# Optimization experiments

Measured on AMD Instinct MI355X. Metric: run time of the kernel, lower is better.

## Reference

```python
import jax, jax.numpy as jnp
import numpy as np

N_NODES = 100000
N_EDGES = 1600000
IN_FEATS = 128
OUT_FEATS = 128


def setup_inputs() -> dict:
    key = jax.random.key(0)
    k1, k2, k3, k4, k5, k6, k7 = jax.random.split(key, 7)
    feat = jax.random.normal(k1, (N_NODES, IN_FEATS), dtype=jnp.float32)
    # positive per-node norms (sqrt-degree-like), shifted away from zero
    in_norm = jax.random.uniform(k2, (N_NODES,), dtype=jnp.float32) + 0.5
    out_norm = jax.random.uniform(k3, (N_NODES,), dtype=jnp.float32) + 0.5
    src = jax.random.randint(k4, (N_EDGES,), 0, N_NODES, dtype=jnp.int32)
    dst = jax.random.randint(k5, (N_EDGES,), 0, N_NODES, dtype=jnp.int32)
    # linear params, uniform(-stdv, stdv) as in reset_parameters
    stdv = 1.0 / np.sqrt(IN_FEATS)
    W = jax.random.uniform(k6, (OUT_FEATS, IN_FEATS), dtype=jnp.float32, minval=-stdv, maxval=stdv)
    b = jax.random.uniform(k7, (OUT_FEATS,), dtype=jnp.float32, minval=-stdv, maxval=stdv)
    return {"feat": feat, "in_norm": in_norm, "out_norm": out_norm,
            "src": src, "dst": dst, "W": W, "b": b}


def reference(feat, in_norm, out_norm, src, dst, W, b):
    # h_u = feat / out_norm  (per source node)
    h = feat / out_norm[:, None]                      # [N, F]
    # copy_u + sum: scatter-add source features into destination nodes
    msgs = h[src]                                     # [E, F] gather
    agg = jax.ops.segment_sum(msgs, dst, num_segments=N_NODES)  # [N, F]
    # normalize by in_norm, then linear
    out = (agg / in_norm[:, None]) @ W.T + b          # [N, F_out]
    return out
```

## Files before the change

kernel.cpp:

```cpp
#include <hip/hip_runtime.h>

#define N_NODES 100000
#define N_EDGES 1600000
#define F 128
#define NB2 391
#define BSZ 256
#define CHUNK 4000
#define NBLK_BIN 400
#define CAP2 5440
#define NGROUP 6250

#define WS_V7 32627712

typedef __attribute__((ext_vector_type(8))) short short8;
typedef __attribute__((ext_vector_type(4))) float f32x4;

__device__ __forceinline__ unsigned short f2bf(float f) {
    unsigned u = __float_as_uint(f);
    return (unsigned short)((u + 0x7fffu + ((u >> 16) & 1u)) >> 16);
}

__global__ __launch_bounds__(256) void prep_chist_kernel(
    const float* __restrict__ feat, const float* __restrict__ out_norm,
    const int* __restrict__ dst,
    unsigned short* __restrict__ h, int* __restrict__ base_t)
{
    __shared__ int c[NB2];
    const int t = threadIdx.x;
    const bool do_hist = (blockIdx.x < NBLK_BIN);
    if (do_hist) {
        for (int i = t; i < NB2; i += 256) c[i] = 0;
        __syncthreads();
    }
    int q = blockIdx.x * 256 + t;
    int row = q >> 5;
    float r = 1.0f / out_norm[row];
    float4 v = ((const float4*)feat)[q];
    ushort4 o;
    o.x = f2bf(v.x * r); o.y = f2bf(v.y * r);
    o.z = f2bf(v.z * r); o.w = f2bf(v.w * r);
    ((ushort4*)h)[q] = o;
    if (do_hist) {
        int e0 = blockIdx.x * CHUNK;
        for (int i = t; i < CHUNK; i += 256)
            atomicAdd(&c[dst[e0 + i] >> 8], 1);
        __syncthreads();
        for (int i = t; i < NB2; i += 256)
            base_t[i * NBLK_BIN + blockIdx.x] = c[i];
    }
}

__global__ __launch_bounds__(64) void cscan1_kernel(
    int* __restrict__ base_t, int* __restrict__ btot)
{
    int b = blockIdx.x, l = threadIdx.x;
    int carry = 0;
    #pragma unroll
    for (int r = 0; r < 7; ++r) {
        int idx = r * 64 + l;
        bool ok = idx < NBLK_BIN;
        int v = ok ? base_t[b * NBLK_BIN + idx] : 0;
        int incl = v;
        #pragma unroll
        for (int off = 1; off < 64; off <<= 1) {
            int n = __shfl_up(incl, off);
            if (l >= off) incl += n;
        }
        if (ok) base_t[b * NBLK_BIN + idx] = incl - v + carry;
        carry += __shfl(incl, 63);
    }
    if (l == 0) btot[b] = carry;
}

__global__ __launch_bounds__(512) void binscatter_kernel(
    const int* __restrict__ src, const int* __restrict__ dst,
    const int* __restrict__ base_t, const int* __restrict__ btot,
    int* __restrict__ pool)
{
    __shared__ int cba[NB2];
    __shared__ int sm[512];
    int t = threadIdx.x, blk = blockIdx.x;
    int v = (t < NB2) ? btot[t] : 0;
    sm[t] = v;
    __syncthreads();
    for (int off = 1; off < 512; off <<= 1) {
        int x = (t >= off) ? sm[t - off] : 0;
        __syncthreads();
        sm[t] += x;
        __syncthreads();
    }
    if (t < NB2) cba[t] = (sm[t] - v) + base_t[t * NBLK_BIN + blk];
    __syncthreads();
    int e0 = blk * CHUNK;
    for (int i = t; i < CHUNK; i += 512) {
        int d = dst[e0 + i];
        int s = src[e0 + i];
        int b = d >> 8;
        int pos = atomicAdd(&cba[b], 1);
        pool[pos] = ((d & 255) << 17) | s;
    }
}

__global__ __launch_bounds__(1024) void fsort_gather_kernel(
    const int* __restrict__ pool, const int* __restrict__ btot,
    const unsigned short* __restrict__ h, const float* __restrict__ in_norm,
    float* __restrict__ agg)
{
    __shared__ int pairs[CAP2];
    __shared__ int sorted_s[CAP2];
    __shared__ int fcnt[BSZ];
    __shared__ int s0[BSZ];
    __shared__ int sexcl[BSZ];
    __shared__ int wsum[4];
    __shared__ int woff[4];
    __shared__ int sbeg[1];

    const int t = threadIdx.x, b = blockIdx.x;
    const int lane = t & 63, wv = t >> 6;

    if (t < 64) {
        int acc = 0;
        for (int j = t; j < NB2; j += 64) acc += (j < b) ? btot[j] : 0;
        #pragma unroll
        for (int off = 32; off; off >>= 1) acc += __shfl_xor(acc, off);
        if (t == 0) sbeg[0] = acc;
    }
    if (t < BSZ) fcnt[t] = 0;
    __syncthreads();
    const int beg = sbeg[0];
    int cnt = btot[b];
    if (cnt > CAP2) cnt = CAP2;

    for (int i = t; i < cnt; i += 1024) pairs[i] = pool[beg + i];
    __syncthreads();
    for (int i = t; i < cnt; i += 1024) atomicAdd(&fcnt[pairs[i] >> 17], 1);
    __syncthreads();

    if (t < BSZ) {
        int v = fcnt[t];
        int incl = v;
        #pragma unroll
        for (int off = 1; off < 64; off <<= 1) {
            int n = __shfl_up(incl, off);
            if (lane >= off) incl += n;
        }
        s0[t] = incl;
        if (lane == 63) wsum[wv] = incl;
    }
    __syncthreads();
    if (t < 64) {
        int v = (t < 4) ? wsum[t] : 0;
        int incl = v;
        #pragma unroll
        for (int off = 1; off < 4; off <<= 1) {
            int n = __shfl_up(incl, off);
            if (lane >= off) incl += n;
        }
        if (t < 4) woff[t] = incl - v;
    }
    __syncthreads();
    if (t < BSZ) {
        int sv = s0[t] + woff[t >> 6];
        s0[t] = sv;
        sexcl[t] = sv - fcnt[t];
    }
    __syncthreads();

    for (int i = t; i < cnt; i += 1024) {
        int p = pairs[i];
        int pos = atomicAdd(&sexcl[p >> 17], 1);
        sorted_s[pos] = p & 0x1FFFF;
    }
    __syncthreads();

    const unsigned* hp = (const unsigned*)h;
    const int node0 = b << 8;
    const int nEnd = wv * 16 + 16;
    for (int nl = wv * 16; nl < nEnd; ++nl) {
        const int node = node0 + nl;
        if (node >= N_NODES) break;
        const int start = (nl == 0) ? 0 : s0[nl - 1];
        const int end = s0[nl];
        float ax = 0.f, ay = 0.f;
        int e = start;
        for (; e + 7 < end; e += 8) {
            unsigned u0 = hp[(size_t)sorted_s[e]     * 64 + lane];
            unsigned u1 = hp[(size_t)sorted_s[e + 1] * 64 + lane];
            unsigned u2 = hp[(size_t)sorted_s[e + 2] * 64 + lane];
            unsigned u3 = hp[(size_t)sorted_s[e + 3] * 64 + lane];
            unsigned u4 = hp[(size_t)sorted_s[e + 4] * 64 + lane];
            unsigned u5 = hp[(size_t)sorted_s[e + 5] * 64 + lane];
            unsigned u6 = hp[(size_t)sorted_s[e + 6] * 64 + lane];
            unsigned u7 = hp[(size_t)sorted_s[e + 7] * 64 + lane];
            ax += __uint_as_float(u0 << 16) + __uint_as_float(u1 << 16)
                + __uint_as_float(u2 << 16) + __uint_as_float(u3 << 16)
                + __uint_as_float(u4 << 16) + __uint_as_float(u5 << 16)
                + __uint_as_float(u6 << 16) + __uint_as_float(u7 << 16);
            ay += __uint_as_float(u0 & 0xffff0000u) + __uint_as_float(u1 & 0xffff0000u)
                + __uint_as_float(u2 & 0xffff0000u) + __uint_as_float(u3 & 0xffff0000u)
                + __uint_as_float(u4 & 0xffff0000u) + __uint_as_float(u5 & 0xffff0000u)
                + __uint_as_float(u6 & 0xffff0000u) + __uint_as_float(u7 & 0xffff0000u);
        }
        for (; e + 3 < end; e += 4) {
            unsigned u0 = hp[(size_t)sorted_s[e]     * 64 + lane];
            unsigned u1 = hp[(size_t)sorted_s[e + 1] * 64 + lane];
            unsigned u2 = hp[(size_t)sorted_s[e + 2] * 64 + lane];
            unsigned u3 = hp[(size_t)sorted_s[e + 3] * 64 + lane];
            ax += __uint_as_float(u0 << 16) + __uint_as_float(u1 << 16)
                + __uint_as_float(u2 << 16) + __uint_as_float(u3 << 16);
            ay += __uint_as_float(u0 & 0xffff0000u) + __uint_as_float(u1 & 0xffff0000u)
                + __uint_as_float(u2 & 0xffff0000u) + __uint_as_float(u3 & 0xffff0000u);
        }
        for (; e < end; ++e) {
            unsigned u = hp[(size_t)sorted_s[e] * 64 + lane];
            ax += __uint_as_float(u << 16);
            ay += __uint_as_float(u & 0xffff0000u);
        }
        const float rin = 1.0f / in_norm[node];
        float2 o; o.x = ax * rin; o.y = ay * rin;
        ((float2*)agg)[(size_t)node * 64 + lane] = o;
    }
}

__global__ __launch_bounds__(256) void transform_mfma_kernel(
    float* __restrict__ out, const float* __restrict__ W,
    const float* __restrict__ bias)
{
    __shared__ short Wb[F * F];
    const int t = threadIdx.x;
    #pragma unroll
    for (int i = 0; i < 8; ++i) {
        int c = t + i * 256;
        int n = c >> 4, kc = c & 15;
        const float4* wp = (const float4*)(W + n * F + kc * 8);
        float4 w0 = wp[0], w1 = wp[1];
        short8 v;
        v[0] = (short)f2bf(w0.x); v[1] = (short)f2bf(w0.y);
        v[2] = (short)f2bf(w0.z); v[3] = (short)f2bf(w0.w);
        v[4] = (short)f2bf(w1.x); v[5] = (short)f2bf(w1.y);
        v[6] = (short)f2bf(w1.z); v[7] = (short)f2bf(w1.w);
        *(short8*)&Wb[n * F + ((kc ^ (n & 15)) * 8)] = v;
    }
    __syncthreads();

    const int wave = t >> 6, lane = t & 63;
    const int wblk = blockIdx.x * 4 + wave;
    if (wblk >= NGROUP) return;
    const int r0 = wblk * 16;
    const int m = lane & 15, q = lane >> 4;
    const float4* arow = (const float4*)(out + (size_t)(r0 + m) * F);

    short8 afrag[4];
    #pragma unroll
    for (int s = 0; s < 4; ++s) {
        int k0 = s * 32 + q * 8;
        float4 x0 = arow[k0 >> 2];
        float4 x1 = arow[(k0 >> 2) + 1];
        short8 a;
        a[0] = (short)f2bf(x0.x); a[1] = (short)f2bf(x0.y);
        a[2] = (short)f2bf(x0.z); a[3] = (short)f2bf(x0.w);
        a[4] = (short)f2bf(x1.x); a[5] = (short)f2bf(x1.y);
        a[6] = (short)f2bf(x1.z); a[7] = (short)f2bf(x1.w);
        afrag[s] = a;
    }

    f32x4 acc[8];
    #pragma unroll
    for (int c = 0; c < 8; ++c) { f32x4 z = {0.f, 0.f, 0.f, 0.f}; acc[c] = z; }

    #pragma unroll
    for (int s = 0; s < 4; ++s) {
        const int kc = s * 4 + q;
        #pragma unroll
        for (int c = 0; c < 8; ++c) {
            const int n = c * 16 + m;
            short8 bfrag = *(const short8*)&Wb[n * F + ((kc ^ m) * 8)];
            acc[c] = __builtin_amdgcn_mfma_f32_16x16x32_bf16(
                afrag[s], bfrag, acc[c], 0, 0, 0);
        }
    }

    #pragma unroll
    for (int c = 0; c < 8; ++c) {
        const float bc = bias[c * 16 + m];
        #pragma unroll
        for (int r = 0; r < 4; ++r) {
            out[(size_t)(r0 + q * 4 + r) * F + c * 16 + m] = acc[c][r] + bc;
        }
    }
}

__global__ __launch_bounds__(256) void scatter_kernel(
    const float* __restrict__ feat, const float* __restrict__ out_norm,
    const int* __restrict__ src, const int* __restrict__ dst,
    float* __restrict__ agg)
{
    const int wave = threadIdx.x >> 6;
    const int lane = threadIdx.x & 63;
    const int e = blockIdx.x * 4 + wave;
    const int s = src[e];
    const int d = dst[e];
    const float rn = 1.0f / out_norm[s];
    const float2 v = ((const float2*)(feat + (size_t)s * F))[lane];
    float* ap = agg + (size_t)d * F + lane * 2;
    unsafeAtomicAdd(ap,     v.x * rn);
    unsafeAtomicAdd(ap + 1, v.y * rn);
}

__global__ __launch_bounds__(256) void transform_kernel(
    float* __restrict__ out, const float* __restrict__ in_norm,
    const float* __restrict__ W, const float* __restrict__ bias)
{
    __shared__ float Wt[F * F];
    const int t = threadIdx.x;
    #pragma unroll
    for (int i = 0; i < (F * F) / 256; ++i) {
        int idx = t + i * 256;
        int j = idx >> 7;
        int k = idx & (F - 1);
        Wt[k * F + j] = W[idx];
    }
    __syncthreads();
    const int wave = t >> 6, lane = t & 63;
    const float b0 = bias[lane];
    const float b1 = bias[lane + 64];
    const int ngroups = N_NODES / 16;
    for (int g = blockIdx.x; g < ngroups; g += gridDim.x) {
        const int r = g * 16 + wave * 4;
        const float4* a0 = (const float4*)(out + (size_t)r * F);
        const float4* a1 = a0 + F / 4;
        const float4* a2 = a0 + 2 * (F / 4);
        const float4* a3 = a0 + 3 * (F / 4);
        float acc00 = 0.f, acc01 = 0.f, acc10 = 0.f, acc11 = 0.f;
        float acc20 = 0.f, acc21 = 0.f, acc30 = 0.f, acc31 = 0.f;
        for (int k4 = 0; k4 < F / 4; ++k4) {
            const float4 x0 = a0[k4]; const float4 x1 = a1[k4];
            const float4 x2 = a2[k4]; const float4 x3 = a3[k4];
            const float xs0[4] = {x0.x, x0.y, x0.z, x0.w};
            const float xs1[4] = {x1.x, x1.y, x1.z, x1.w};
            const float xs2[4] = {x2.x, x2.y, x2.z, x2.w};
            const float xs3[4] = {x3.x, x3.y, x3.z, x3.w};
            #pragma unroll
            for (int kk = 0; kk < 4; ++kk) {
                const int k = k4 * 4 + kk;
                const float w0 = Wt[k * F + lane];
                const float w1 = Wt[k * F + 64 + lane];
                acc00 = fmaf(xs0[kk], w0, acc00); acc01 = fmaf(xs0[kk], w1, acc01);
                acc10 = fmaf(xs1[kk], w0, acc10); acc11 = fmaf(xs1[kk], w1, acc11);
                acc20 = fmaf(xs2[kk], w0, acc20); acc21 = fmaf(xs2[kk], w1, acc21);
                acc30 = fmaf(xs3[kk], w0, acc30); acc31 = fmaf(xs3[kk], w1, acc31);
            }
        }
        const float i0 = 1.0f / in_norm[r + 0];
        const float i1 = 1.0f / in_norm[r + 1];
        const float i2 = 1.0f / in_norm[r + 2];
        const float i3 = 1.0f / in_norm[r + 3];
        out[(size_t)(r + 0) * F + lane]      = acc00 * i0 + b0;
        out[(size_t)(r + 0) * F + 64 + lane] = acc01 * i0 + b1;
        out[(size_t)(r + 1) * F + lane]      = acc10 * i1 + b0;
        out[(size_t)(r + 1) * F + 64 + lane] = acc11 * i1 + b1;
        out[(size_t)(r + 2) * F + lane]      = acc20 * i2 + b0;
        out[(size_t)(r + 2) * F + 64 + lane] = acc21 * i2 + b1;
        out[(size_t)(r + 3) * F + lane]      = acc30 * i3 + b0;
        out[(size_t)(r + 3) * F + 64 + lane] = acc31 * i3 + b1;
    }
}

extern "C" void kernel_launch(void* const* d_in, const int* in_sizes, int n_in,
                              void* d_out, int out_size, void* d_ws, size_t ws_size,
                              hipStream_t stream) {
    const float* feat     = (const float*)d_in[0];
    const float* in_norm  = (const float*)d_in[1];
    const float* out_norm = (const float*)d_in[2];
    const int*   src      = (const int*)d_in[3];
    const int*   dst      = (const int*)d_in[4];
    const float* W        = (const float*)d_in[5];
    const float* b        = (const float*)d_in[6];
    float* out = (float*)d_out;

    if (ws_size >= (size_t)WS_V7) {
        char* w = (char*)d_ws;
        int*            pool   = (int*)(w + 0);
        int*            base_t = (int*)(w + 6400000);
        int*            btot   = (int*)(w + 7025600);
        unsigned short* h      = (unsigned short*)(w + 7027712);

        prep_chist_kernel<<<(N_NODES * 32) / 256, 256, 0, stream>>>(
            feat, out_norm, dst, h, base_t);
        cscan1_kernel<<<NB2, 64, 0, stream>>>(base_t, btot);
        binscatter_kernel<<<NBLK_BIN, 512, 0, stream>>>(src, dst, base_t, btot, pool);
        fsort_gather_kernel<<<NB2, 1024, 0, stream>>>(pool, btot, h, in_norm, out);
        transform_mfma_kernel<<<(NGROUP + 3) / 4, 256, 0, stream>>>(out, W, b);
    } else {
        hipMemsetAsync(out, 0, (size_t)N_NODES * F * sizeof(float), stream);
        scatter_kernel<<<N_EDGES / 4, 256, 0, stream>>>(feat, out_norm, src, dst, out);
        transform_kernel<<<2048, 256, 0, stream>>>(out, in_norm, W, b);
    }
}
```

Baseline: 229.7 us.

## Apply linear transform before aggregation and fuse it into the prep kernel

Because the linear layer commutes with the per-node sum, the change multiplies the scaled source features by W (MFMA, bf16) inside the prep/histogram kernel and stores the transformed rows as bf16. The gather kernel then sums transformed rows, scales by in_norm and adds the bias, writing the final output directly. This removes the separate transform kernel and its read and write of the full fp32 aggregate. In exchange the prep kernel carries 32KB of LDS for W and does the GEMM work there, and the output rounding now happens before aggregation.

```diff
diff --git a/kernel.cpp b/kernel.cpp
--- a/kernel.cpp
+++ b/kernel.cpp
@@ -9,8 +9,9 @@
 #define NBLK_BIN 400
 #define CAP2 5440
 #define NGROUP 6250
-
-#define WS_V7 32627712
+#define NPREP_BLK 1563
+
+#define WS_V8 32627712
 
 typedef __attribute__((ext_vector_type(8))) short short8;
 typedef __attribute__((ext_vector_type(4))) float f32x4;
@@ -20,31 +21,88 @@
     return (unsigned short)((u + 0x7fffu + ((u >> 16) & 1u)) >> 16);
 }
 
-__global__ __launch_bounds__(256) void prep_chist_kernel(
+__global__ __launch_bounds__(256) void prep_gemm_chist_kernel(
     const float* __restrict__ feat, const float* __restrict__ out_norm,
-    const int* __restrict__ dst,
-    unsigned short* __restrict__ h, int* __restrict__ base_t)
-{
+    const int* __restrict__ dst, const float* __restrict__ W,
+    unsigned short* __restrict__ g, int* __restrict__ base_t)
+{
+    __shared__ short Wb[F * F];
     __shared__ int c[NB2];
     const int t = threadIdx.x;
     const bool do_hist = (blockIdx.x < NBLK_BIN);
     if (do_hist) {
         for (int i = t; i < NB2; i += 256) c[i] = 0;
-        __syncthreads();
-    }
-    int q = blockIdx.x * 256 + t;
-    int row = q >> 5;
-    float r = 1.0f / out_norm[row];
-    float4 v = ((const float4*)feat)[q];
-    ushort4 o;
-    o.x = f2bf(v.x * r); o.y = f2bf(v.y * r);
-    o.z = f2bf(v.z * r); o.w = f2bf(v.w * r);
-    ((ushort4*)h)[q] = o;
+    }
+    #pragma unroll
+    for (int i = 0; i < 8; ++i) {
+        int cc = t + i * 256;
+        int n = cc >> 4, kc = cc & 15;
+        const float4* wp = (const float4*)(W + n * F + kc * 8);
+        float4 w0 = wp[0], w1 = wp[1];
+        short8 v;
+        v[0] = (short)f2bf(w0.x); v[1] = (short)f2bf(w0.y);
+        v[2] = (short)f2bf(w0.z); v[3] = (short)f2bf(w0.w);
+        v[4] = (short)f2bf(w1.x); v[5] = (short)f2bf(w1.y);
+        v[6] = (short)f2bf(w1.z); v[7] = (short)f2bf(w1.w);
+        *(short8*)&Wb[n * F + ((kc ^ (n & 15)) * 8)] = v;
+    }
+    __syncthreads();
+
     if (do_hist) {
         int e0 = blockIdx.x * CHUNK;
         for (int i = t; i < CHUNK; i += 256)
             atomicAdd(&c[dst[e0 + i] >> 8], 1);
-        __syncthreads();
+    }
+
+    const int wave = t >> 6, lane = t & 63;
+    const int wblk = blockIdx.x * 4 + wave;
+    if (wblk < NGROUP) {
+        const int r0 = wblk * 16;
+        const int m = lane & 15, q = lane >> 4;
+        const float* arow = feat + (size_t)(r0 + m) * F;
+        const float rscale = 1.0f / out_norm[r0 + m];
+
+        short8 afrag[4];
+        #pragma unroll
+        for (int s = 0; s < 4; ++s) {
+            int k0 = s * 32 + q * 8;
+            float4 x0 = *(const float4*)(arow + k0);
+            float4 x1 = *(const float4*)(arow + k0 + 4);
+            short8 a;
+            a[0] = (short)f2bf(x0.x * rscale); a[1] = (short)f2bf(x0.y * rscale);
+            a[2] = (short)f2bf(x0.z * rscale); a[3] = (short)f2bf(x0.w * rscale);
+            a[4] = (short)f2bf(x1.x * rscale); a[5] = (short)f2bf(x1.y * rscale);
+            a[6] = (short)f2bf(x1.z * rscale); a[7] = (short)f2bf(x1.w * rscale);
+            afrag[s] = a;
+        }
+
+        f32x4 acc[8];
+        #pragma unroll
+        for (int cc = 0; cc < 8; ++cc) { f32x4 z = {0.f, 0.f, 0.f, 0.f}; acc[cc] = z; }
+
+        #pragma unroll
+        for (int s = 0; s < 4; ++s) {
+            const int kc = s * 4 + q;
+            #pragma unroll
+            for (int cc = 0; cc < 8; ++cc) {
+                const int n = cc * 16 + m;
+                short8 bfrag = *(const short8*)&Wb[n * F + ((kc ^ m) * 8)];
+                acc[cc] = __builtin_amdgcn_mfma_f32_16x16x32_bf16(
+                    afrag[s], bfrag, acc[cc], 0, 0, 0);
+            }
+        }
+
+        #pragma unroll
+        for (int cc = 0; cc < 8; ++cc) {
+            #pragma unroll
+            for (int r = 0; r < 4; ++r) {
+                g[(size_t)(r0 + q * 4 + r) * F + cc * 16 + m] = f2bf(acc[cc][r]);
+            }
+        }
+    }
+
+    __syncthreads();
+    if (do_hist) {
         for (int i = t; i < NB2; i += 256)
             base_t[i * NBLK_BIN + blockIdx.x] = c[i];
     }
@@ -103,8 +161,8 @@
 
 __global__ __launch_bounds__(1024) void fsort_gather_kernel(
     const int* __restrict__ pool, const int* __restrict__ btot,
-    const unsigned short* __restrict__ h, const float* __restrict__ in_norm,
-    float* __restrict__ agg)
+    const unsigned short* __restrict__ g, const float* __restrict__ in_norm,
+    const float* __restrict__ bias, float* __restrict__ out)
 {
     __shared__ int pairs[CAP2];
     __shared__ int sorted_s[CAP2];
@@ -173,7 +231,8 @@
     }
     __syncthreads();
 
-    const unsigned* hp = (const unsigned*)h;
+    const unsigned* gp = (const unsigned*)g;
+    const float2 bl = ((const float2*)bias)[lane];
     const int node0 = b << 8;
     const int nEnd = wv * 16 + 16;
     for (int nl = wv * 16; nl < nEnd; ++nl) {
@@ -184,14 +243,14 @@
         float ax = 0.f, ay = 0.f;
         int e = start;
         for (; e + 7 < end; e += 8) {
-            unsigned u0 = hp[(size_t)sorted_s[e]     * 64 + lane];
-            unsigned u1 = hp[(size_t)sorted_s[e + 1] * 64 + lane];
-            unsigned u2 = hp[(size_t)sorted_s[e + 2] * 64 + lane];
-            unsigned u3 = hp[(size_t)sorted_s[e + 3] * 64 + lane];
-            unsigned u4 = hp[(size_t)sorted_s[e + 4] * 64 + lane];
-            unsigned u5 = hp[(size_t)sorted_s[e + 5] * 64 + lane];
-            unsigned u6 = hp[(size_t)sorted_s[e + 6] * 64 + lane];
-            unsigned u7 = hp[(size_t)sorted_s[e + 7] * 64 + lane];
+            unsigned u0 = gp[(size_t)sorted_s[e]     * 64 + lane];
+            unsigned u1 = gp[(size_t)sorted_s[e + 1] * 64 + lane];
+            unsigned u2 = gp[(size_t)sorted_s[e + 2] * 64 + lane];
+            unsigned u3 = gp[(size_t)sorted_s[e + 3] * 64 + lane];
+            unsigned u4 = gp[(size_t)sorted_s[e + 4] * 64 + lane];
+            unsigned u5 = gp[(size_t)sorted_s[e + 5] * 64 + lane];
+            unsigned u6 = gp[(size_t)sorted_s[e + 6] * 64 + lane];
+            unsigned u7 = gp[(size_t)sorted_s[e + 7] * 64 + lane];
             ax += __uint_as_float(u0 << 16) + __uint_as_float(u1 << 16)
                 + __uint_as_float(u2 << 16) + __uint_as_float(u3 << 16)
                 + __uint_as_float(u4 << 16) + __uint_as_float(u5 << 16)
@@ -202,91 +261,23 @@
                 + __uint_as_float(u6 & 0xffff0000u) + __uint_as_float(u7 & 0xffff0000u);
         }
         for (; e + 3 < end; e += 4) {
-            unsigned u0 = hp[(size_t)sorted_s[e]     * 64 + lane];
-            unsigned u1 = hp[(size_t)sorted_s[e + 1] * 64 + lane];
-            unsigned u2 = hp[(size_t)sorted_s[e + 2] * 64 + lane];
-            unsigned u3 = hp[(size_t)sorted_s[e + 3] * 64 + lane];
+            unsigned u0 = gp[(size_t)sorted_s[e]     * 64 + lane];
+            unsigned u1 = gp[(size_t)sorted_s[e + 1] * 64 + lane];
+            unsigned u2 = gp[(size_t)sorted_s[e + 2] * 64 + lane];
+            unsigned u3 = gp[(size_t)sorted_s[e + 3] * 64 + lane];
             ax += __uint_as_float(u0 << 16) + __uint_as_float(u1 << 16)
                 + __uint_as_float(u2 << 16) + __uint_as_float(u3 << 16);
             ay += __uint_as_float(u0 & 0xffff0000u) + __uint_as_float(u1 & 0xffff0000u)
                 + __uint_as_float(u2 & 0xffff0000u) + __uint_as_float(u3 & 0xffff0000u);
         }
         for (; e < end; ++e) {
-            unsigned u = hp[(size_t)sorted_s[e] * 64 + lane];
+            unsigned u = gp[(size_t)sorted_s[e] * 64 + lane];
             ax += __uint_as_float(u << 16);
             ay += __uint_as_float(u & 0xffff0000u);
         }
         const float rin = 1.0f / in_norm[node];
-        float2 o; o.x = ax * rin; o.y = ay * rin;
-        ((float2*)agg)[(size_t)node * 64 + lane] = o;
-    }
-}
-
-__global__ __launch_bounds__(256) void transform_mfma_kernel(
-    float* __restrict__ out, const float* __restrict__ W,
-    const float* __restrict__ bias)
-{
-    __shared__ short Wb[F * F];
-    const int t = threadIdx.x;
-    #pragma unroll
-    for (int i = 0; i < 8; ++i) {
-        int c = t + i * 256;
-        int n = c >> 4, kc = c & 15;
-        const float4* wp = (const float4*)(W + n * F + kc * 8);
-        float4 w0 = wp[0], w1 = wp[1];
-        short8 v;
-        v[0] = (short)f2bf(w0.x); v[1] = (short)f2bf(w0.y);
-        v[2] = (short)f2bf(w0.z); v[3] = (short)f2bf(w0.w);
-        v[4] = (short)f2bf(w1.x); v[5] = (short)f2bf(w1.y);
-        v[6] = (short)f2bf(w1.z); v[7] = (short)f2bf(w1.w);
-        *(short8*)&Wb[n * F + ((kc ^ (n & 15)) * 8)] = v;
-    }
-    __syncthreads();
-
-    const int wave = t >> 6, lane = t & 63;
-    const int wblk = blockIdx.x * 4 + wave;
-    if (wblk >= NGROUP) return;
-    const int r0 = wblk * 16;
-    const int m = lane & 15, q = lane >> 4;
-    const float4* arow = (const float4*)(out + (size_t)(r0 + m) * F);
-
-    short8 afrag[4];
-    #pragma unroll
-    for (int s = 0; s < 4; ++s) {
-        int k0 = s * 32 + q * 8;
-        float4 x0 = arow[k0 >> 2];
-        float4 x1 = arow[(k0 >> 2) + 1];
-        short8 a;
-        a[0] = (short)f2bf(x0.x); a[1] = (short)f2bf(x0.y);
-        a[2] = (short)f2bf(x0.z); a[3] = (short)f2bf(x0.w);
-        a[4] = (short)f2bf(x1.x); a[5] = (short)f2bf(x1.y);
-        a[6] = (short)f2bf(x1.z); a[7] = (short)f2bf(x1.w);
-        afrag[s] = a;
-    }
-
-    f32x4 acc[8];
-    #pragma unroll
-    for (int c = 0; c < 8; ++c) { f32x4 z = {0.f, 0.f, 0.f, 0.f}; acc[c] = z; }
-
-    #pragma unroll
-    for (int s = 0; s < 4; ++s) {
-        const int kc = s * 4 + q;
-        #pragma unroll
-        for (int c = 0; c < 8; ++c) {
-            const int n = c * 16 + m;
-            short8 bfrag = *(const short8*)&Wb[n * F + ((kc ^ m) * 8)];
-            acc[c] = __builtin_amdgcn_mfma_f32_16x16x32_bf16(
-                afrag[s], bfrag, acc[c], 0, 0, 0);
-        }
-    }
-
-    #pragma unroll
-    for (int c = 0; c < 8; ++c) {
-        const float bc = bias[c * 16 + m];
-        #pragma unroll
-        for (int r = 0; r < 4; ++r) {
-            out[(size_t)(r0 + q * 4 + r) * F + c * 16 + m] = acc[c][r] + bc;
-        }
+        float2 o; o.x = ax * rin + bl.x; o.y = ay * rin + bl.y;
+        ((float2*)out)[(size_t)node * 64 + lane] = o;
     }
 }
 
@@ -325,8 +316,8 @@
     const float b0 = bias[lane];
     const float b1 = bias[lane + 64];
     const int ngroups = N_NODES / 16;
-    for (int g = blockIdx.x; g < ngroups; g += gridDim.x) {
-        const int r = g * 16 + wave * 4;
+    for (int gi = blockIdx.x; gi < ngroups; gi += gridDim.x) {
+        const int r = gi * 16 + wave * 4;
         const float4* a0 = (const float4*)(out + (size_t)r * F);
         const float4* a1 = a0 + F / 4;
         const float4* a2 = a0 + 2 * (F / 4);
@@ -378,19 +369,18 @@
     const float* b        = (const float*)d_in[6];
     float* out = (float*)d_out;
 
-    if (ws_size >= (size_t)WS_V7) {
+    if (ws_size >= (size_t)WS_V8) {
         char* w = (char*)d_ws;
         int*            pool   = (int*)(w + 0);
         int*            base_t = (int*)(w + 6400000);
         int*            btot   = (int*)(w + 7025600);
-        unsigned short* h      = (unsigned short*)(w + 7027712);
-
-        prep_chist_kernel<<<(N_NODES * 32) / 256, 256, 0, stream>>>(
-            feat, out_norm, dst, h, base_t);
+        unsigned short* g      = (unsigned short*)(w + 7027712);
+
+        prep_gemm_chist_kernel<<<NPREP_BLK, 256, 0, stream>>>(
+            feat, out_norm, dst, W, g, base_t);
         cscan1_kernel<<<NB2, 64, 0, stream>>>(base_t, btot);
         binscatter_kernel<<<NBLK_BIN, 512, 0, stream>>>(src, dst, base_t, btot, pool);
-        fsort_gather_kernel<<<NB2, 1024, 0, stream>>>(pool, btot, h, in_norm, out);
-        transform_mfma_kernel<<<(NGROUP + 3) / 4, 256, 0, stream>>>(out, W, b);
+        fsort_gather_kernel<<<NB2, 1024, 0, stream>>>(pool, btot, g, in_norm, b, out);
     } else {
         hipMemsetAsync(out, 0, (size_t)N_NODES * F * sizeof(float), stream);
         scatter_kernel<<<N_EDGES / 4, 256, 0, stream>>>(feat, out_norm, src, dst, out);
```

Result: faster. 215.8 us (-6.1%).
